# Kernel optimization log

Measured on AMD Instinct MI355X. Metric: run time of the kernel, lower is better.

The kernel has to match this reference:

```python
import jax, jax.numpy as jnp
import numpy as np

# channels_choice from the module: [8,16,24,32,40,48,56,64]
CH = jnp.arange(8, 72, 8)
EPS = 1e-5

def _masks():
    # [8,64] binary masks: mask[i, ch] = 1 if ch < channels_choice[i]
    return (jnp.arange(64)[None, :] < CH[:, None]).astype(jnp.float32)

def _bn(x, axes):
    # BatchNorm, affine=False, track_running_stats=False -> batch statistics
    mu = jnp.mean(x, axes, keepdims=True)
    var = jnp.var(x, axes, keepdims=True)
    return (x - mu) * jax.lax.rsqrt(var + EPS)

def _conv3(x, w):
    return jax.lax.conv_general_dilated(x, w, (1, 1), 'SAME',
                                        dimension_numbers=('NCHW', 'OIHW', 'NCHW'))

def _nor_conv(x, w1, w2, a1, a2):
    # Entangled two-part nor_conv edge.
    # p1: relu -> conv3x3 -> bn, mixture over 8 output-channel widths. Slicing
    # output channels + zero-pad + alpha-weighted sum collapses (BN is per-channel)
    # to a soft channel mask m1.
    masks = _masks()                      # [8,64]
    m1 = masks.T @ a1                     # [64] soft output-channel mask
    h = _bn(_conv3(jax.nn.relu(x), w1), (0, 2, 3)) * m1[None, :, None, None]
    # p2: conv3x3 -> bn, mixture over 8 input-channel widths. BN is nonlinear, so
    # the 8 candidates are genuinely computed (vectorized on a leading axis).
    xs = h[None] * masks[:, None, :, None, None]   # [8,B,64,H,W]
    K, B, C, H, W = xs.shape
    y = _conv3(xs.reshape(K * B, C, H, W), w2).reshape(K, B, C, H, W)
    y = _bn(y, (1, 3, 4))
    return jnp.einsum('k,kbchw->bchw', a2, y)

def _avg_pool3(x):
    # AvgPool2d(3, stride=1, padding=1, count_include_pad=False)
    s = jax.lax.reduce_window(x, 0.0, jax.lax.add, (1, 1, 3, 3), (1, 1, 1, 1), 'SAME')
    cnt = jax.lax.reduce_window(jnp.ones((1, 1) + x.shape[2:], x.dtype), 0.0,
                                jax.lax.add, (1, 1, 3, 3), (1, 1, 1, 1), 'SAME')
    return s / cnt

def _combi_mask(a1, a2):
    # combi=True mixture over itertools.product(channels, channels) with weights
    # a1[i]*a2[j]; for channelwise ops (skip/pool) slicing in to c_i then out to c_j
    # keeps channels < min(c_i,c_j), so the double sum factorizes into m1*m2.
    masks = _masks()
    return (masks.T @ a1) * (masks.T @ a2)

def _cell(inputs, alphas1, alphas2, W1_0, W2_0, W1_1, W2_1, W1_4, W2_4, W1_5, W2_5):
    cm = _combi_mask(alphas1, alphas2)[None, :, None, None]
    # genotype: 1<-(conv~0) | 2<-(conv~0, avgpool~1) | 3<-(skip~0, conv~1, conv~2)
    n1 = _nor_conv(inputs, W1_0, W2_0, alphas1, alphas2)
    n2 = _nor_conv(inputs, W1_1, W2_1, alphas1, alphas2) + _avg_pool3(n1) * cm
    n3 = (inputs * cm
          + _nor_conv(n1, W1_4, W2_4, alphas1, alphas2)
          + _nor_conv(n2, W1_5, W2_5, alphas1, alphas2))
    return n3

def setup_inputs():
    key = jax.random.key(0)
    ks = jax.random.split(key, 12)
    B, C, H, W = 64, 64, 32, 32
    a1 = jax.random.uniform(ks[1], (8,), jnp.float32)
    a2 = jax.random.uniform(ks[2], (8,), jnp.float32)
    d = {
        'inputs': jax.random.normal(ks[0], (B, C, H, W), jnp.float32),
        'alphas1': a1 / a1.sum(),
        'alphas2': a2 / a2.sum(),
    }
    wscale = 0.05  # ~ 1/sqrt(64*9) fan-in init
    for i, name in enumerate(['W1_0', 'W2_0', 'W1_1', 'W2_1', 'W1_4', 'W2_4', 'W1_5', 'W2_5']):
        d[name] = jax.random.normal(ks[3 + i], (64, 64, 3, 3), jnp.float32) * wscale
    return d

def reference(inputs, alphas1, alphas2, W1_0, W2_0, W1_1, W2_1, W1_4, W2_4, W1_5, W2_5):
    return _cell(inputs, alphas1, alphas2, W1_0, W2_0, W1_1, W2_1, W1_4, W2_4, W1_5, W2_5)
```

## Files before the change

kernel.cpp:

```cpp
#include <hip/hip_runtime.h>

#define EPS 1e-5f
#define NRED 65536.0f
#define IMST 73984
#define PATCH 8704
#define PATCH6 13056

typedef short bf16x8 __attribute__((ext_vector_type(8)));
typedef float f32x4 __attribute__((ext_vector_type(4)));
typedef unsigned short u16;

#define MFMA16(a, b, c) __builtin_amdgcn_mfma_f32_16x16x32_bf16(a, b, c, 0, 0, 0)
#define SWZ(px, oct) ((px) * 64 + (((oct) ^ ((px) & 7)) * 8))

__device__ __forceinline__ u16 f2bf(float x) {
  union { float f; unsigned u; } v; v.f = x;
  unsigned r = v.u + 0x7FFF + ((v.u >> 16) & 1);
  return (u16)(r >> 16);
}
__device__ __forceinline__ float bf2f(u16 h) {
  union { unsigned u; float f; } v; v.u = ((unsigned)h) << 16;
  return v.f;
}
__device__ __forceinline__ unsigned pk2(float a, float b) {
  return (unsigned)f2bf(a) | ((unsigned)f2bf(b) << 16);
}

template <int CTRL>
__device__ __forceinline__ float dpp_mov(float x) {
  int xi = __builtin_bit_cast(int, x);
  int r = __builtin_amdgcn_update_dpp(0, xi, CTRL, 0xF, 0xF, true);
  return __builtin_bit_cast(float, r);
}
__device__ __forceinline__ float row_reduce16(float x) {
  x += dpp_mov<0x111>(x);
  x += dpp_mov<0x112>(x);
  x += dpp_mov<0x114>(x);
  x += dpp_mov<0x118>(x);
  return x;
}

__device__ __forceinline__ void stage_mask(const u16* __restrict__ src,
                                           u16* __restrict__ shp, int tid, int R0) {
#pragma unroll
  for (int i = 0; i < 5; ++i) {
    int c = i * 256 + tid;
    if (i == 4 && tid >= 64) break;
    int px = c >> 3, oct = c & 7;
    int prow = px / 34, pcol = px - prow * 34;
    bool halo = (R0 + prow == 0) || (R0 + prow == 33) || (pcol == 0) || (pcol == 33);
    uint4 v = {0u, 0u, 0u, 0u};
    if (!halo) v = *(const uint4*)&src[(size_t)c * 8];
    *(uint4*)&shp[SWZ(px, oct)] = v;
  }
}

__device__ __forceinline__ void stage_affine(const u16* __restrict__ src,
                                             u16* __restrict__ shp, int tid, int R0,
                                             const float* __restrict__ stE) {
  const int oct0 = tid & 7;
  float s[8], bb[8];
#pragma unroll
  for (int j = 0; j < 8; ++j) { s[j] = stE[oct0 * 8 + j]; bb[j] = stE[64 + oct0 * 8 + j]; }
#pragma unroll
  for (int i = 0; i < 5; ++i) {
    int c = i * 256 + tid;
    if (i == 4 && tid >= 64) break;
    int px = c >> 3, oct = c & 7;
    int prow = px / 34, pcol = px - prow * 34;
    bool halo = (R0 + prow == 0) || (R0 + prow == 33) || (pcol == 0) || (pcol == 33);
    uint4 o = {0u, 0u, 0u, 0u};
    if (!halo) {
      uint4 u = *(const uint4*)&src[(size_t)c * 8];
      unsigned uv[4] = {u.x, u.y, u.z, u.w};
      unsigned rv[4];
#pragma unroll
      for (int p2 = 0; p2 < 4; ++p2) {
        float lo = bf2f((u16)(uv[p2] & 0xffff)) * s[p2 * 2] + bb[p2 * 2];
        float hi = bf2f((u16)(uv[p2] >> 16)) * s[p2 * 2 + 1] + bb[p2 * 2 + 1];
        rv[p2] = pk2(lo, hi);
      }
      o.x = rv[0]; o.y = rv[1]; o.z = rv[2]; o.w = rv[3];
    }
    *(uint4*)&shp[SWZ(px, oct)] = o;
  }
}


__global__ __launch_bounds__(256) void prep_k(
    const float* __restrict__ x, u16* __restrict__ xT, u16* __restrict__ n1T,
    const float* __restrict__ w10, const float* __restrict__ w11,
    const float* __restrict__ w12, const float* __restrict__ w13,
    const float* __restrict__ w20, const float* __restrict__ w21,
    const float* __restrict__ w22, const float* __restrict__ w23,
    u16* __restrict__ wT1, u16* __restrict__ wG64, u16* __restrict__ wT8) {
  __shared__ __align__(16) u16 sh[64 * 72];
  const int bid = blockIdx.x;
  const int tid = threadIdx.x;
  if (bid < 36) {
    int e = bid / 9, tap = bid % 9;
    const float* w = e == 0 ? w10 : e == 1 ? w11 : e == 2 ? w12 : w13;
    u16* dst = wT1 + e * 36864 + tap * 4096;
    for (int idx = tid; idx < 4096; idx += 256) {
      int co = idx >> 6, ci = idx & 63;
      dst[idx] = f2bf(w[(co * 64 + ci) * 9 + tap]);
    }
  } else if (bid < 324) {
    int r = bid - 36;
    int e = r / 72, bx = r % 72;
    const float* w = e == 0 ? w20 : e == 1 ? w21 : e == 2 ? w22 : w23;
    int g, tap;
    u16* dst;
    if (bx < 64) { g = bx >> 3; tap = bx & 7; dst = wG64 + e * 32768 + bx * 512; }
    else         { g = bx - 64; tap = 8;      dst = wT8 + e * 4096 + g * 512; }
    for (int idx = tid; idx < 512; idx += 256) {
      int co = idx >> 3, cig = idx & 7;
      dst[idx] = f2bf(w[(co * 64 + g * 8 + cig) * 9 + tap]);
    }
  } else if (bid < 388) {
    int b = bid - 324;
    if (tid >= 132) return;
    int R, C;
    if (tid < 34) { R = 0; C = tid; }
    else if (tid < 68) { R = 33; C = tid - 34; }
    else if (tid < 100) { R = tid - 67; C = 0; }
    else { R = tid - 99; C = 33; }
    u16* p = n1T + (size_t)b * IMST + (size_t)(R * 34 + C) * 64;
    uint4 z = {0u, 0u, 0u, 0u};
#pragma unroll
    for (int i = 0; i < 8; ++i) *(uint4*)&p[i * 8] = z;
  } else {
    const int bb = bid - 388;
    const int b = bb >> 4, slab = bb & 15;
    const int ln = tid & 63, w = tid >> 6;
    const float* xb = x + (size_t)b * 65536 + slab * 64;
#pragma unroll
    for (int i = 0; i < 16; ++i) {
      int ci = w + i * 4;
      float v = xb[ci * 1024 + ln];
      sh[ln * 72 + ci] = f2bf(fmaxf(v, 0.f));
    }
    __syncthreads();
    u16* dst = xT + (size_t)b * IMST;
#pragma unroll
    for (int j = 0; j < 2; ++j) {
      int idx = tid + j * 256;
      int p = idx >> 3, oct = idx & 7;
      int gp = slab * 64 + p;
      int R = gp >> 5, C = gp & 31;
      *(uint4*)&dst[((R + 1) * 34 + C + 1) * 64 + oct * 8] = *(const uint4*)&sh[p * 72 + oct * 8];
    }
  }
}

__global__ __launch_bounds__(256, 4) void convA_k(const u16* __restrict__ in0,
                                                  const u16* __restrict__ in1,
                                                  const u16* __restrict__ wTa,
                                                  const u16* __restrict__ wTb,
                                                  u16* __restrict__ t0,
                                                  u16* __restrict__ t1,
                                                  float* __restrict__ pA) {
  __shared__ __align__(16) u16 shp[PATCH];
  __shared__ float sA[64], qA[64];
  const int tid = threadIdx.x;
  const int b = blockIdx.y, R0 = blockIdx.x * 2, z = blockIdx.z;
  const u16* xin = z ? in1 : in0;
  const u16* wT = z ? wTb : wTa;
  u16* t = z ? t1 : t0;
  if (tid < 64) { sA[tid] = 0.f; qA[tid] = 0.f; }
  stage_mask(xin + (size_t)b * IMST + (size_t)R0 * 2176, shp, tid, R0);
  const int lane = tid & 63, w = tid >> 6;
  const int ln = lane & 15, quad = lane >> 4;
  const int lr = w >> 1, mh = w & 1;
  const u16* wbase = wT + (size_t)((mh * 2) * 16 + ln) * 64 + quad * 8;
  __syncthreads();
  f32x4 acc[2][2];
#pragma unroll
  for (int m2 = 0; m2 < 2; ++m2)
#pragma unroll
    for (int nf = 0; nf < 2; ++nf) acc[m2][nf] = (f32x4){0.f, 0.f, 0.f, 0.f};
#pragma unroll 3
  for (int tap = 0; tap < 9; ++tap) {
    const int dy = tap / 3, dx = tap % 3;
    const int px0 = (lr + dy) * 34 + ln + dx;
    bf16x8 A[2][2];
#pragma unroll
    for (int m2 = 0; m2 < 2; ++m2)
#pragma unroll
      for (int h = 0; h < 2; ++h)
        A[m2][h] = *(const bf16x8*)&wbase[(size_t)(tap * 64 + m2 * 16) * 64 + h * 32];
#pragma unroll
    for (int h = 0; h < 2; ++h) {
      const int oct = h * 4 + quad;
      bf16x8 b0 = *(const bf16x8*)&shp[SWZ(px0, oct)];
      bf16x8 b1 = *(const bf16x8*)&shp[SWZ(px0 + 16, oct)];
      acc[0][0] = MFMA16(A[0][h], b0, acc[0][0]);
      acc[0][1] = MFMA16(A[0][h], b1, acc[0][1]);
      acc[1][0] = MFMA16(A[1][h], b0, acc[1][0]);
      acc[1][1] = MFMA16(A[1][h], b1, acc[1][1]);
    }
  }
  const int R = R0 + lr;
#pragma unroll
  for (int m2 = 0; m2 < 2; ++m2) {
    const int cob = (mh * 2 + m2) * 16 + quad * 4;
#pragma unroll
    for (int nf = 0; nf < 2; ++nf) {
      u16* tb = t + (size_t)b * IMST + (size_t)((R + 1) * 34 + nf * 16 + ln + 1) * 64 + cob;
      uint2 pk;
      pk.x = pk2(acc[m2][nf][0], acc[m2][nf][1]);
      pk.y = pk2(acc[m2][nf][2], acc[m2][nf][3]);
      *(uint2*)tb = pk;
    }
#pragma unroll
    for (int r = 0; r < 4; ++r) {
      float v0 = acc[m2][0][r], v1 = acc[m2][1][r];
      float s = row_reduce16(v0) + row_reduce16(v1);
      float q = row_reduce16(v0 * v0) + row_reduce16(v1 * v1);
      if (ln == 15) {
        atomicAdd(&sA[cob + r], s);
        atomicAdd(&qA[cob + r], q);
      }
    }
  }
  __syncthreads();
  const int blk = z * 1024 + blockIdx.y * 16 + blockIdx.x;
  if (tid < 64) pA[blk * 128 + tid] = sA[tid];
  else if (tid < 128) pA[blk * 128 + tid] = qA[tid - 64];
}

__global__ __launch_bounds__(256) void reducerA_k(const float* __restrict__ pA,
                                                  const float* __restrict__ a1,
                                                  float* __restrict__ stBase) {
  const int tid = threadIdx.x, c = blockIdx.x, z = blockIdx.y;
  const float* pAe = pA + (size_t)z * 1024 * 128;
  float s = 0.f, q = 0.f;
  for (int i = tid; i < 1024; i += 256) {
    s += pAe[i * 128 + c];
    q += pAe[i * 128 + 64 + c];
  }
#pragma unroll
  for (int off = 32; off; off >>= 1) { s += __shfl_xor(s, off); q += __shfl_xor(q, off); }
  __shared__ float red[8];
  int wv = tid >> 6;
  if ((tid & 63) == 0) { red[wv] = s; red[4 + wv] = q; }
  __syncthreads();
  if (tid == 0) {
    float S = red[0] + red[1] + red[2] + red[3];
    float Q = red[4] + red[5] + red[6] + red[7];
    int g = c >> 3;
    float m = 0.f;
    for (int i = g; i < 8; ++i) m += a1[i];
    float mu = S * (1.f / NRED);
    float var = Q * (1.f / NRED) - mu * mu;
    float r = rsqrtf(var + EPS);
    float* stE = stBase + z * 2048;
    stE[c] = r * m;
    stE[64 + c] = -mu * r * m;
  }
}

__global__ __launch_bounds__(512, 4) void convC_k(const u16* __restrict__ t0,
                                                  const u16* __restrict__ t1,
                                                  const u16* __restrict__ wG64,
                                                  const u16* __restrict__ wT8,
                                                  const float* __restrict__ stBase,
                                                  float* __restrict__ pC) {
  __shared__ __align__(16) u16 shp[PATCH6];
  __shared__ __align__(16) u16 shA[64 * 16 * 8];
  __shared__ __align__(16) u16 shA2[8 * 16 * 8];
  __shared__ float sC[4][128], qC[4][128];
  const int tid = threadIdx.x;
  const int b = blockIdx.y, R0 = blockIdx.x * 4;
  const int edge = blockIdx.z;
  const u16* t = edge ? t1 : t0;
  const float* stE = stBase + edge * 2048;
  const u16* wGe = wG64 + edge * 32768;
  const u16* wT8e = wT8 + edge * 4096;
  ((float*)sC)[tid] = 0.f;
  ((float*)qC)[tid] = 0.f;
  {
    const int oct0 = tid & 7;
    float sc[8], bc[8];
#pragma unroll
    for (int j = 0; j < 8; ++j) { sc[j] = stE[oct0 * 8 + j]; bc[j] = stE[64 + oct0 * 8 + j]; }
    const u16* src = t + (size_t)b * IMST + (size_t)R0 * 2176;
#pragma unroll
    for (int i = 0; i < 4; ++i) {
      int c = i * 512 + tid;
      if (i == 3 && tid >= 96) break;
      int px = c >> 3, oct = c & 7;
      int prow = px / 34, pcol = px - prow * 34;
      bool halo = (R0 + prow == 0) || (R0 + prow == 33) || (pcol == 0) || (pcol == 33);
      uint4 o = {0u, 0u, 0u, 0u};
      if (!halo) {
        uint4 u = *(const uint4*)&src[(size_t)c * 8];
        unsigned uv[4] = {u.x, u.y, u.z, u.w};
        unsigned rv[4];
#pragma unroll
        for (int p2 = 0; p2 < 4; ++p2) {
          float lo = bf2f((u16)(uv[p2] & 0xffff)) * sc[p2 * 2] + bc[p2 * 2];
          float hi = bf2f((u16)(uv[p2] >> 16)) * sc[p2 * 2 + 1] + bc[p2 * 2 + 1];
          rv[p2] = pk2(lo, hi);
        }
        o.x = rv[0]; o.y = rv[1]; o.z = rv[2]; o.w = rv[3];
      }
      *(uint4*)&shp[SWZ(px, oct)] = o;
    }
  }
#pragma unroll
  for (int i = 0; i < 2; ++i) {
    int c = i * 512 + tid;
    int row = c >> 4, col = c & 15;
    *(uint4*)&shA[c * 8] = *(const uint4*)&wGe[(size_t)(row * 64 + col) * 8];
  }
  if (tid < 128) {
    int g = tid >> 4, col = tid & 15;
    *(uint4*)&shA2[tid * 8] = *(const uint4*)&wT8e[(size_t)(g * 64 + col) * 8];
  }
  __syncthreads();
  const int lane = tid & 63, w = tid >> 6;
  const int ln = lane & 15, quad = lane >> 4;
  const int lrow = w >> 1, colbase = (w & 1) * 16;
  int px[3];
#pragma unroll
  for (int ch = 0; ch < 3; ++ch) {
    int tp = ch * 4 + quad; if (tp > 8) tp = 8;
    px[ch] = (lrow + tp / 3) * 34 + colbase + ln + tp % 3;
  }
#pragma unroll 1
  for (int coq = 0; coq < 4; ++coq) {
    uint4 wr0, wr1, wr2;
    if (coq < 3) {
      const int nq = coq + 1;
      {
        int c = tid;
        wr0 = *(const uint4*)&wGe[(size_t)((c >> 4) * 64 + nq * 16 + (c & 15)) * 8];
      }
      {
        int c = 512 + tid;
        wr1 = *(const uint4*)&wGe[(size_t)((c >> 4) * 64 + nq * 16 + (c & 15)) * 8];
      }
      if (tid < 128)
        wr2 = *(const uint4*)&wT8e[(size_t)((tid >> 4) * 64 + nq * 16 + (tid & 15)) * 8];
    }
    f32x4 acc[8];
#pragma unroll
    for (int g = 0; g < 8; ++g) acc[g] = (f32x4){0.f, 0.f, 0.f, 0.f};
#pragma unroll
    for (int g = 0; g < 8; ++g) {
#pragma unroll
      for (int ch = 0; ch < 3; ++ch) {
        bf16x8 bx = *(const bf16x8*)&shp[SWZ(px[ch], g)];
        bf16x8 aw;
        if (ch < 2) {
          aw = *(const bf16x8*)&shA[((g * 8 + ch * 4 + quad) * 16 + ln) * 8];
        } else {
          aw = (bf16x8){0, 0, 0, 0, 0, 0, 0, 0};
          if (quad == 0) aw = *(const bf16x8*)&shA2[(g * 16 + ln) * 8];
        }
        acc[g] = MFMA16(aw, bx, acc[g]);
      }
    }
    f32x4 P = (f32x4){0.f, 0.f, 0.f, 0.f};
#pragma unroll
    for (int k = 0; k < 8; ++k) {
      P += acc[k];
#pragma unroll
      for (int r = 0; r < 4; ++r) {
        float v = P[r];
        float s = row_reduce16(v);
        float q = row_reduce16(v * v);
        if (ln == 15) {
          atomicAdd(&sC[coq][k * 16 + quad * 4 + r], s);
          atomicAdd(&qC[coq][k * 16 + quad * 4 + r], q);
        }
      }
    }
    __syncthreads();
    if (coq < 3) {
      *(uint4*)&shA[(size_t)tid * 8] = wr0;
      *(uint4*)&shA[(size_t)(512 + tid) * 8] = wr1;
      if (tid < 128) *(uint4*)&shA2[tid * 8] = wr2;
      __syncthreads();
    }
  }
  __syncthreads();
  const int blk = blockIdx.y * 8 + blockIdx.x;
#pragma unroll 1
  for (int coq = 0; coq < 4; ++coq) {
    const size_t base = ((size_t)(edge * 4 + coq) * 512 + blk) * 256;
    if (tid < 128) pC[base + tid] = sC[coq][tid];
    else if (tid < 256) pC[base + 128 + (tid - 128)] = qC[coq][tid - 128];
  }
}

__global__ __launch_bounds__(256) void redCprepE_k(const float* __restrict__ pC,
                                                   const float* __restrict__ w2a,
                                                   const float* __restrict__ w2b,
                                                   const float* __restrict__ a1,
                                                   const float* __restrict__ a2,
                                                   float* __restrict__ stBase,
                                                   u16* __restrict__ wEbase,
                                                   float* __restrict__ cm) {
  const int tid = threadIdx.x, c = blockIdx.x, z = blockIdx.y;
  const int coq = c >> 4, cl = c & 15;
  const float* w2 = z ? w2b : w2a;
  float* stE = stBase + z * 2048;
  u16* wE = wEbase + z * 36864;
  float s[8], q[8];
#pragma unroll
  for (int k = 0; k < 8; ++k) { s[k] = 0.f; q[k] = 0.f; }
  for (int i = tid; i < 512; i += 256) {
    const float* pb = pC + ((size_t)(z * 4 + coq) * 512 + i) * 256;
#pragma unroll
    for (int k = 0; k < 8; ++k) {
      s[k] += pb[k * 16 + cl];
      q[k] += pb[128 + k * 16 + cl];
    }
  }
#pragma unroll
  for (int k = 0; k < 8; ++k) {
#pragma unroll
    for (int off = 32; off; off >>= 1) { s[k] += __shfl_xor(s[k], off); q[k] += __shfl_xor(q[k], off); }
  }
  __shared__ float red[4][16];
  __shared__ float gL[8];
  int wv = tid >> 6;
  if ((tid & 63) == 0) {
#pragma unroll
    for (int k = 0; k < 8; ++k) { red[wv][k * 2] = s[k]; red[wv][k * 2 + 1] = q[k]; }
  }
  __syncthreads();
  if (tid == 0) {
    float suf = 0.f, bias = 0.f;
    for (int k = 7; k >= 0; --k) {
      float S = red[0][k * 2] + red[1][k * 2] + red[2][k * 2] + red[3][k * 2];
      float Q = red[0][k * 2 + 1] + red[1][k * 2 + 1] + red[2][k * 2 + 1] + red[3][k * 2 + 1];
      float mu = S * (1.f / NRED);
      float var = Q * (1.f / NRED) - mu * mu;
      float rr = rsqrtf(var + EPS);
      bias -= a2[k] * mu * rr;
      suf += a2[k] * rr;
      gL[k] = suf;
    }
    stE[128 + c] = bias;
    if (z == 0) {
      int g = c >> 3;
      float m1 = 0.f, m2 = 0.f;
      for (int i = g; i < 8; ++i) { m1 += a1[i]; m2 += a2[i]; }
      cm[c] = m1 * m2;
    }
  }
  __syncthreads();
  for (int idx = tid; idx < 576; idx += 256) {
    int tap = idx >> 6, ci = idx & 63;
    wE[(tap * 64 + c) * 64 + ci] = f2bf(w2[(c * 64 + ci) * 9 + tap] * gL[ci >> 3]);
  }
}

template <int MODE>
__global__ __launch_bounds__(256, 4) void convE_k(const u16* __restrict__ t,
                                                  const float* __restrict__ stE,
                                                  const u16* __restrict__ wEp,
                                                  u16* __restrict__ d1,
                                                  u16* __restrict__ d2,
                                                  const float* __restrict__ cm) {
  __shared__ __align__(16) u16 shp[PATCH];
  __shared__ __align__(16) u16 shn[MODE == 1 ? PATCH : 8];
  __shared__ float cmL[64], biasL[64];
  const int tid = threadIdx.x;
  const int b = blockIdx.y, R0 = blockIdx.x * 2;
  if (tid < 64) { cmL[tid] = cm[tid]; biasL[tid] = stE[128 + tid]; }
  stage_affine(t + (size_t)b * IMST + (size_t)R0 * 2176, shp, tid, R0, stE);
  if constexpr (MODE == 1) {
    const u16* nsrc = d2 + (size_t)b * IMST + (size_t)R0 * 2176;
#pragma unroll
    for (int i = 0; i < 5; ++i) {
      int c = i * 256 + tid;
      if (i == 4 && tid >= 64) break;
      int px = c >> 3, oct = c & 7;
      *(uint4*)&shn[SWZ(px, oct)] = *(const uint4*)&nsrc[(size_t)c * 8];
    }
  }
  const int lane = tid & 63, w = tid >> 6;
  const int ln = lane & 15, quad = lane >> 4;
  const int lr = w >> 1, mh = w & 1;
  const u16* wbase = wEp + (size_t)((mh * 2) * 16 + ln) * 64 + quad * 8;
  __syncthreads();
  f32x4 acc[2][2];
#pragma unroll
  for (int m2 = 0; m2 < 2; ++m2)
#pragma unroll
    for (int nf = 0; nf < 2; ++nf) acc[m2][nf] = (f32x4){0.f, 0.f, 0.f, 0.f};
#pragma unroll 3
  for (int tap = 0; tap < 9; ++tap) {
    const int dy = tap / 3, dx = tap % 3;
    const int px0 = (lr + dy) * 34 + ln + dx;
    bf16x8 A[2][2];
#pragma unroll
    for (int m2 = 0; m2 < 2; ++m2)
#pragma unroll
      for (int h = 0; h < 2; ++h)
        A[m2][h] = *(const bf16x8*)&wbase[(size_t)(tap * 64 + m2 * 16) * 64 + h * 32];
#pragma unroll
    for (int h = 0; h < 2; ++h) {
      const int oct = h * 4 + quad;
      bf16x8 b0 = *(const bf16x8*)&shp[SWZ(px0, oct)];
      bf16x8 b1 = *(const bf16x8*)&shp[SWZ(px0 + 16, oct)];
      acc[0][0] = MFMA16(A[0][h], b0, acc[0][0]);
      acc[0][1] = MFMA16(A[0][h], b1, acc[0][1]);
      acc[1][0] = MFMA16(A[1][h], b0, acc[1][0]);
      acc[1][1] = MFMA16(A[1][h], b1, acc[1][1]);
    }
  }
  const int R = R0 + lr;
#pragma unroll
  for (int m2 = 0; m2 < 2; ++m2) {
    const int cob = (mh * 2 + m2) * 16 + quad * 4;
#pragma unroll
    for (int nf = 0; nf < 2; ++nf) {
      const int C = nf * 16 + ln;
      const size_t haloPx = (size_t)b * IMST + (size_t)((R + 1) * 34 + C + 1) * 64 + cob;
      float v[4];
#pragma unroll
      for (int r = 0; r < 4; ++r) v[r] = acc[m2][nf][r] + biasL[cob + r];
      if (MODE == 0) {
        uint2 pk, pkr;
        pk.x = pk2(v[0], v[1]); pk.y = pk2(v[2], v[3]);
        pkr.x = pk2(fmaxf(v[0], 0.f), fmaxf(v[1], 0.f));
        pkr.y = pk2(fmaxf(v[2], 0.f), fmaxf(v[3], 0.f));
        *(uint2*)&d1[haloPx] = pk;
        *(uint2*)&d2[haloPx] = pkr;
      } else {
        float ps[4] = {0.f, 0.f, 0.f, 0.f};
#pragma unroll
        for (int dy = 0; dy < 3; ++dy)
#pragma unroll
          for (int dx = 0; dx < 3; ++dx) {
            const int ppx = (lr + dy) * 34 + C + dx;
            uint2 u = *(const uint2*)&shn[SWZ(ppx, cob >> 3) + (cob & 7)];
            ps[0] += bf2f((u16)(u.x & 0xffff));
            ps[1] += bf2f((u16)(u.x >> 16));
            ps[2] += bf2f((u16)(u.y & 0xffff));
            ps[3] += bf2f((u16)(u.y >> 16));
          }
        float rows = 3.f - (R == 0 ? 1.f : 0.f) - (R == 31 ? 1.f : 0.f);
        float cols = 3.f - (C == 0 ? 1.f : 0.f) - (C == 31 ? 1.f : 0.f);
        float inv = 1.f / (rows * cols);
        uint2 pkr;
        float t0v = fmaxf(v[0] + ps[0] * inv * cmL[cob], 0.f);
        float t1v = fmaxf(v[1] + ps[1] * inv * cmL[cob + 1], 0.f);
        float t2v = fmaxf(v[2] + ps[2] * inv * cmL[cob + 2], 0.f);
        float t3v = fmaxf(v[3] + ps[3] * inv * cmL[cob + 3], 0.f);
        pkr.x = pk2(t0v, t1v); pkr.y = pk2(t2v, t3v);
        *(uint2*)&d1[haloPx] = pkr;
      }
    }
  }
}

__global__ __launch_bounds__(256, 4) void convE23_k(const u16* __restrict__ t0,
                                                    const u16* __restrict__ t1,
                                                    const float* __restrict__ stBase,
                                                    const u16* __restrict__ wE2,
                                                    const u16* __restrict__ wE3,
                                                    float* __restrict__ outp,
                                                    const float* __restrict__ x,
                                                    const float* __restrict__ cm) {
  __shared__ __align__(16) u16 shp2[2 * PATCH];
  __shared__ float cmL[64], biasL[64];
  const int tid = threadIdx.x;
  const int b = blockIdx.y, R0 = blockIdx.x * 2;
  if (tid < 64) {
    cmL[tid] = cm[tid];
    biasL[tid] = stBase[128 + tid] + stBase[2048 + 128 + tid];
  }
  stage_affine(t0 + (size_t)b * IMST + (size_t)R0 * 2176, shp2, tid, R0, stBase);
  stage_affine(t1 + (size_t)b * IMST + (size_t)R0 * 2176, shp2 + PATCH, tid, R0, stBase + 2048);
  __syncthreads();
  const int lane = tid & 63, w = tid >> 6;
  const int ln = lane & 15, quad = lane >> 4;
  const int lr = w >> 1, mh = w & 1;
  f32x4 acc[2][2];
#pragma unroll
  for (int m2 = 0; m2 < 2; ++m2)
#pragma unroll
    for (int nf = 0; nf < 2; ++nf) acc[m2][nf] = (f32x4){0.f, 0.f, 0.f, 0.f};
#pragma unroll 1
  for (int ei = 0; ei < 2; ++ei) {
    const u16* wEp = ei ? wE3 : wE2;
    const u16* sp = &shp2[ei * PATCH];
    const u16* wbase = wEp + (size_t)((mh * 2) * 16 + ln) * 64 + quad * 8;
#pragma unroll 3
    for (int tap = 0; tap < 9; ++tap) {
      const int dy = tap / 3, dx = tap % 3;
      const int px0 = (lr + dy) * 34 + ln + dx;
      bf16x8 A[2][2];
#pragma unroll
      for (int m2 = 0; m2 < 2; ++m2)
#pragma unroll
        for (int h = 0; h < 2; ++h)
          A[m2][h] = *(const bf16x8*)&wbase[(size_t)(tap * 64 + m2 * 16) * 64 + h * 32];
#pragma unroll
      for (int h = 0; h < 2; ++h) {
        const int oct = h * 4 + quad;
        bf16x8 b0 = *(const bf16x8*)&sp[SWZ(px0, oct)];
        bf16x8 b1 = *(const bf16x8*)&sp[SWZ(px0 + 16, oct)];
        acc[0][0] = MFMA16(A[0][h], b0, acc[0][0]);
        acc[0][1] = MFMA16(A[0][h], b1, acc[0][1]);
        acc[1][0] = MFMA16(A[1][h], b0, acc[1][0]);
        acc[1][1] = MFMA16(A[1][h], b1, acc[1][1]);
      }
    }
  }
  const int R = R0 + lr;
#pragma unroll
  for (int m2 = 0; m2 < 2; ++m2) {
    const int cob = (mh * 2 + m2) * 16 + quad * 4;
#pragma unroll
    for (int nf = 0; nf < 2; ++nf) {
      const int C = nf * 16 + ln;
      size_t base = (size_t)b * 65536 + (size_t)cob * 1024 + R * 32 + C;
#pragma unroll
      for (int r = 0; r < 4; ++r)
        outp[base + (size_t)r * 1024] =
            acc[m2][nf][r] + biasL[cob + r] + x[base + (size_t)r * 1024] * cmL[cob + r];
    }
  }
}

extern "C" void kernel_launch(void* const* d_in, const int* in_sizes, int n_in,
                              void* d_out, int out_size, void* d_ws, size_t ws_size,
                              hipStream_t stream) {
  const float* x  = (const float*)d_in[0];
  const float* a1 = (const float*)d_in[1];
  const float* a2 = (const float*)d_in[2];
  const float* W1[4] = {(const float*)d_in[3], (const float*)d_in[5],
                        (const float*)d_in[7], (const float*)d_in[9]};
  const float* W2[4] = {(const float*)d_in[4], (const float*)d_in[6],
                        (const float*)d_in[8], (const float*)d_in[10]};
  float* out = (float*)d_out;
  char* ws = (char*)d_ws;
  const size_t HB = (size_t)IMST * 64 * 2;
  u16* xT  = (u16*)ws;
  u16* t0  = (u16*)(ws + HB);
  u16* t1  = (u16*)(ws + 2 * HB);
  u16* n1T = (u16*)(ws + 3 * HB);
  u16* n1r = (u16*)(ws + 4 * HB);
  u16* n2r = (u16*)(ws + 5 * HB);
  char* p = ws + 6 * HB;
  float* st  = (float*)p;            p += 8256 * 4;
  u16* wT1   = (u16*)p;              p += 4 * 36864 * 2;
  u16* wG64  = (u16*)p;              p += 4 * 32768 * 2;
  u16* wT8   = (u16*)p;              p += 4 * 4096 * 2;
  u16* wE    = (u16*)p;              p += 4 * 36864 * 2;
  float* pA  = (float*)p;            p += 2 * 1024 * 128 * 4;
  float* pC  = (float*)p;
  float* cm  = st + 8192;

  prep_k<<<1412, 256, 0, stream>>>(x, xT, n1T,
                                   W1[0], W1[1], W1[2], W1[3],
                                   W2[0], W2[1], W2[2], W2[3],
                                   wT1, wG64, wT8);

  dim3 gA(16, 64, 2), gC(8, 64, 2), gE(16, 64);
  convA_k<<<gA, 256, 0, stream>>>(xT, xT, wT1, wT1 + 36864, t0, t1, pA);
  reducerA_k<<<dim3(64, 2), 256, 0, stream>>>(pA, a1, st);
  convC_k<<<gC, 512, 0, stream>>>(t0, t1, wG64, wT8, st, pC);
  redCprepE_k<<<dim3(64, 2), 256, 0, stream>>>(pC, W2[0], W2[1], a1, a2, st, wE, cm);
  convE_k<0><<<gE, 256, 0, stream>>>(t0, st, wE, n1T, n1r, cm);
  convE_k<1><<<gE, 256, 0, stream>>>(t1, st + 2048, wE + 36864, n2r, n1T, cm);
  convA_k<<<gA, 256, 0, stream>>>(n1r, n2r, wT1 + 2 * 36864, wT1 + 3 * 36864, t0, t1, pA);
  reducerA_k<<<dim3(64, 2), 256, 0, stream>>>(pA, a1, st + 4096);
  convC_k<<<gC, 512, 0, stream>>>(t0, t1, wG64 + 2 * 32768, wT8 + 2 * 4096, st + 4096, pC);
  redCprepE_k<<<dim3(64, 2), 256, 0, stream>>>(pC, W2[2], W2[3], a1, a2, st + 4096,
                                               wE + 2 * 36864, cm);
  convE23_k<<<gE, 256, 0, stream>>>(t0, t1, st + 4096, wE + 2 * 36864, wE + 3 * 36864,
                                    out, x, cm);
}
```

Baseline: 423.4 us.

## Fuse n1 and n2 convE stages, recomputing n1 halo rows in shared memory

Merges the two convE launches into one kernel. Each block now computes the raw n1 output for its two rows plus one halo row above and below, keeps it in shared memory, and uses it directly for the avg-pool term of n2. This drops the n1T global round trip, the n1T halo zeroing in prep, and one kernel launch. The cost is redundant conv work on the halo rows, which doubles the MFMA work for the n1 part, plus larger shared memory that lowers occupancy from 4 to 3 blocks per SIMD.

Measured after the change: 449.4 us. 6.2% more time.

```diff
diff --git a/kernel.cpp b/kernel.cpp
--- a/kernel.cpp
+++ b/kernel.cpp
@@ -88,7 +88,7 @@
 
 
 __global__ __launch_bounds__(256) void prep_k(
-    const float* __restrict__ x, u16* __restrict__ xT, u16* __restrict__ n1T,
+    const float* __restrict__ x, u16* __restrict__ xT,
     const float* __restrict__ w10, const float* __restrict__ w11,
     const float* __restrict__ w12, const float* __restrict__ w13,
     const float* __restrict__ w20, const float* __restrict__ w21,
@@ -117,20 +117,8 @@
       int co = idx >> 3, cig = idx & 7;
       dst[idx] = f2bf(w[(co * 64 + g * 8 + cig) * 9 + tap]);
     }
-  } else if (bid < 388) {
-    int b = bid - 324;
-    if (tid >= 132) return;
-    int R, C;
-    if (tid < 34) { R = 0; C = tid; }
-    else if (tid < 68) { R = 33; C = tid - 34; }
-    else if (tid < 100) { R = tid - 67; C = 0; }
-    else { R = tid - 99; C = 33; }
-    u16* p = n1T + (size_t)b * IMST + (size_t)(R * 34 + C) * 64;
-    uint4 z = {0u, 0u, 0u, 0u};
-#pragma unroll
-    for (int i = 0; i < 8; ++i) *(uint4*)&p[i * 8] = z;
   } else {
-    const int bb = bid - 388;
+    const int bb = bid - 324;
     const int b = bb >> 4, slab = bb & 15;
     const int ln = tid & 63, w = tid >> 6;
     const float* xb = x + (size_t)b * 65536 + slab * 64;
@@ -459,34 +447,122 @@
   }
 }
 
-template <int MODE>
-__global__ __launch_bounds__(256, 4) void convE_k(const u16* __restrict__ t,
-                                                  const float* __restrict__ stE,
-                                                  const u16* __restrict__ wEp,
-                                                  u16* __restrict__ d1,
-                                                  u16* __restrict__ d2,
-                                                  const float* __restrict__ cm) {
-  __shared__ __align__(16) u16 shp[PATCH];
-  __shared__ __align__(16) u16 shn[MODE == 1 ? PATCH : 8];
-  __shared__ float cmL[64], biasL[64];
+__global__ __launch_bounds__(256, 3) void convE01_k(const u16* __restrict__ t0,
+                                                    const u16* __restrict__ t1,
+                                                    const float* __restrict__ stBase,
+                                                    const u16* __restrict__ wE1,
+                                                    const u16* __restrict__ wE2,
+                                                    u16* __restrict__ n1r,
+                                                    u16* __restrict__ n2r,
+                                                    const float* __restrict__ cm) {
+  __shared__ __align__(16) u16 shp6[PATCH6];
+  __shared__ __align__(16) u16 shn[PATCH];
+  __shared__ float cmL[64], b0L[64], b1L[64];
   const int tid = threadIdx.x;
   const int b = blockIdx.y, R0 = blockIdx.x * 2;
-  if (tid < 64) { cmL[tid] = cm[tid]; biasL[tid] = stE[128 + tid]; }
-  stage_affine(t + (size_t)b * IMST + (size_t)R0 * 2176, shp, tid, R0, stE);
-  if constexpr (MODE == 1) {
-    const u16* nsrc = d2 + (size_t)b * IMST + (size_t)R0 * 2176;
-#pragma unroll
-    for (int i = 0; i < 5; ++i) {
+  if (tid < 64) {
+    cmL[tid] = cm[tid];
+    b0L[tid] = stBase[128 + tid];
+    b1L[tid] = stBase[2048 + 128 + tid];
+  }
+  {
+    const int oct0 = tid & 7;
+    float sc[8], bc[8];
+#pragma unroll
+    for (int j = 0; j < 8; ++j) { sc[j] = stBase[oct0 * 8 + j]; bc[j] = stBase[64 + oct0 * 8 + j]; }
+    const int S = R0 - 1;
+    const u16* src = t0 + (size_t)b * IMST + (ptrdiff_t)S * 2176;
+#pragma unroll
+    for (int i = 0; i < 7; ++i) {
       int c = i * 256 + tid;
-      if (i == 4 && tid >= 64) break;
+      if (i == 6 && tid >= 96) break;
       int px = c >> 3, oct = c & 7;
-      *(uint4*)&shn[SWZ(px, oct)] = *(const uint4*)&nsrc[(size_t)c * 8];
+      int prow = px / 34, pcol = px - prow * 34;
+      int ar = S + prow;
+      bool halo = (ar <= 0) || (ar >= 33) || (pcol == 0) || (pcol == 33);
+      uint4 o = {0u, 0u, 0u, 0u};
+      if (!halo) {
+        uint4 u = *(const uint4*)&src[(size_t)c * 8];
+        unsigned uv[4] = {u.x, u.y, u.z, u.w};
+        unsigned rv[4];
+#pragma unroll
+        for (int p2 = 0; p2 < 4; ++p2) {
+          float lo = bf2f((u16)(uv[p2] & 0xffff)) * sc[p2 * 2] + bc[p2 * 2];
+          float hi = bf2f((u16)(uv[p2] >> 16)) * sc[p2 * 2 + 1] + bc[p2 * 2 + 1];
+          rv[p2] = pk2(lo, hi);
+        }
+        o.x = rv[0]; o.y = rv[1]; o.z = rv[2]; o.w = rv[3];
+      }
+      *(uint4*)&shp6[SWZ(px, oct)] = o;
     }
   }
   const int lane = tid & 63, w = tid >> 6;
   const int ln = lane & 15, quad = lane >> 4;
   const int lr = w >> 1, mh = w & 1;
-  const u16* wbase = wEp + (size_t)((mh * 2) * 16 + ln) * 64 + quad * 8;
+  if (tid < 64) {
+    int rr = tid >> 4, colsel = (tid >> 3) & 1, oct = tid & 7;
+    uint4 z = {0u, 0u, 0u, 0u};
+    *(uint4*)&shn[SWZ(rr * 34 + (colsel ? 33 : 0), oct)] = z;
+  }
+  const u16* wb1 = wE1 + (size_t)((mh * 2) * 16 + ln) * 64 + quad * 8;
+  const u16* wb2 = wE2 + (size_t)((mh * 2) * 16 + ln) * 64 + quad * 8;
+  __syncthreads();
+#pragma unroll 1
+  for (int ri = 0; ri < 2; ++ri) {
+    const int nr = 2 * ri + lr;
+    const int orow = R0 - 1 + nr;
+    f32x4 acc[2][2];
+#pragma unroll
+    for (int m2 = 0; m2 < 2; ++m2)
+#pragma unroll
+      for (int nf = 0; nf < 2; ++nf) acc[m2][nf] = (f32x4){0.f, 0.f, 0.f, 0.f};
+#pragma unroll 3
+    for (int tap = 0; tap < 9; ++tap) {
+      const int dy = tap / 3, dx = tap % 3;
+      const int px0 = (nr + dy) * 34 + ln + dx;
+      bf16x8 A[2][2];
+#pragma unroll
+      for (int m2 = 0; m2 < 2; ++m2)
+#pragma unroll
+        for (int h = 0; h < 2; ++h)
+          A[m2][h] = *(const bf16x8*)&wb1[(size_t)(tap * 64 + m2 * 16) * 64 + h * 32];
+#pragma unroll
+      for (int h = 0; h < 2; ++h) {
+        const int oct = h * 4 + quad;
+        bf16x8 b0 = *(const bf16x8*)&shp6[SWZ(px0, oct)];
+        bf16x8 b1 = *(const bf16x8*)&shp6[SWZ(px0 + 16, oct)];
+        acc[0][0] = MFMA16(A[0][h], b0, acc[0][0]);
+        acc[0][1] = MFMA16(A[0][h], b1, acc[0][1]);
+        acc[1][0] = MFMA16(A[1][h], b0, acc[1][0]);
+        acc[1][1] = MFMA16(A[1][h], b1, acc[1][1]);
+      }
+    }
+    const bool valid = (orow >= 0) && (orow <= 31);
+    const bool interior = (nr == 1) || (nr == 2);
+#pragma unroll
+    for (int m2 = 0; m2 < 2; ++m2) {
+      const int cob = (mh * 2 + m2) * 16 + quad * 4;
+#pragma unroll
+      for (int nf = 0; nf < 2; ++nf) {
+        const int C = nf * 16 + ln;
+        float v[4];
+#pragma unroll
+        for (int r = 0; r < 4; ++r) v[r] = acc[m2][nf][r] + b0L[cob + r];
+        uint2 raw;
+        raw.x = pk2(v[0], v[1]); raw.y = pk2(v[2], v[3]);
+        if (!valid) { raw.x = 0u; raw.y = 0u; }
+        *(uint2*)&shn[SWZ(nr * 34 + C + 1, cob >> 3) + (cob & 7)] = raw;
+        if (interior) {
+          uint2 pr;
+          pr.x = pk2(fmaxf(v[0], 0.f), fmaxf(v[1], 0.f));
+          pr.y = pk2(fmaxf(v[2], 0.f), fmaxf(v[3], 0.f));
+          *(uint2*)&n1r[(size_t)b * IMST + (size_t)((orow + 1) * 34 + C + 1) * 64 + cob] = pr;
+        }
+      }
+    }
+  }
+  __syncthreads();
+  stage_affine(t1 + (size_t)b * IMST + (size_t)R0 * 2176, shp6, tid, R0, stBase + 2048);
   __syncthreads();
   f32x4 acc[2][2];
 #pragma unroll
@@ -502,12 +578,12 @@
     for (int m2 = 0; m2 < 2; ++m2)
 #pragma unroll
       for (int h = 0; h < 2; ++h)
-        A[m2][h] = *(const bf16x8*)&wbase[(size_t)(tap * 64 + m2 * 16) * 64 + h * 32];
+        A[m2][h] = *(const bf16x8*)&wb2[(size_t)(tap * 64 + m2 * 16) * 64 + h * 32];
 #pragma unroll
     for (int h = 0; h < 2; ++h) {
       const int oct = h * 4 + quad;
-      bf16x8 b0 = *(const bf16x8*)&shp[SWZ(px0, oct)];
-      bf16x8 b1 = *(const bf16x8*)&shp[SWZ(px0 + 16, oct)];
+      bf16x8 b0 = *(const bf16x8*)&shp6[SWZ(px0, oct)];
+      bf16x8 b1 = *(const bf16x8*)&shp6[SWZ(px0 + 16, oct)];
       acc[0][0] = MFMA16(A[0][h], b0, acc[0][0]);
       acc[0][1] = MFMA16(A[0][h], b1, acc[0][1]);
       acc[1][0] = MFMA16(A[1][h], b0, acc[1][0]);
@@ -524,38 +600,29 @@
       const size_t haloPx = (size_t)b * IMST + (size_t)((R + 1) * 34 + C + 1) * 64 + cob;
       float v[4];
 #pragma unroll
-      for (int r = 0; r < 4; ++r) v[r] = acc[m2][nf][r] + biasL[cob + r];
-      if (MODE == 0) {
-        uint2 pk, pkr;
-        pk.x = pk2(v[0], v[1]); pk.y = pk2(v[2], v[3]);
-        pkr.x = pk2(fmaxf(v[0], 0.f), fmaxf(v[1], 0.f));
-        pkr.y = pk2(fmaxf(v[2], 0.f), fmaxf(v[3], 0.f));
-        *(uint2*)&d1[haloPx] = pk;
-        *(uint2*)&d2[haloPx] = pkr;
-      } else {
-        float ps[4] = {0.f, 0.f, 0.f, 0.f};
-#pragma unroll
-        for (int dy = 0; dy < 3; ++dy)
-#pragma unroll
-          for (int dx = 0; dx < 3; ++dx) {
-            const int ppx = (lr + dy) * 34 + C + dx;
-            uint2 u = *(const uint2*)&shn[SWZ(ppx, cob >> 3) + (cob & 7)];
-            ps[0] += bf2f((u16)(u.x & 0xffff));
-            ps[1] += bf2f((u16)(u.x >> 16));
-            ps[2] += bf2f((u16)(u.y & 0xffff));
-            ps[3] += bf2f((u16)(u.y >> 16));
-          }
-        float rows = 3.f - (R == 0 ? 1.f : 0.f) - (R == 31 ? 1.f : 0.f);
-        float cols = 3.f - (C == 0 ? 1.f : 0.f) - (C == 31 ? 1.f : 0.f);
-        float inv = 1.f / (rows * cols);
-        uint2 pkr;
-        float t0v = fmaxf(v[0] + ps[0] * inv * cmL[cob], 0.f);
-        float t1v = fmaxf(v[1] + ps[1] * inv * cmL[cob + 1], 0.f);
-        float t2v = fmaxf(v[2] + ps[2] * inv * cmL[cob + 2], 0.f);
-        float t3v = fmaxf(v[3] + ps[3] * inv * cmL[cob + 3], 0.f);
-        pkr.x = pk2(t0v, t1v); pkr.y = pk2(t2v, t3v);
-        *(uint2*)&d1[haloPx] = pkr;
-      }
+      for (int r = 0; r < 4; ++r) v[r] = acc[m2][nf][r] + b1L[cob + r];
+      float ps[4] = {0.f, 0.f, 0.f, 0.f};
+#pragma unroll
+      for (int dy = 0; dy < 3; ++dy)
+#pragma unroll
+        for (int dx = 0; dx < 3; ++dx) {
+          const int ppx = (lr + dy) * 34 + C + dx;
+          uint2 u = *(const uint2*)&shn[SWZ(ppx, cob >> 3) + (cob & 7)];
+          ps[0] += bf2f((u16)(u.x & 0xffff));
+          ps[1] += bf2f((u16)(u.x >> 16));
+          ps[2] += bf2f((u16)(u.y & 0xffff));
+          ps[3] += bf2f((u16)(u.y >> 16));
+        }
+      float rows = 3.f - (R == 0 ? 1.f : 0.f) - (R == 31 ? 1.f : 0.f);
+      float cols = 3.f - (C == 0 ? 1.f : 0.f) - (C == 31 ? 1.f : 0.f);
+      float inv = 1.f / (rows * cols);
+      uint2 pkr;
+      float t0v = fmaxf(v[0] + ps[0] * inv * cmL[cob], 0.f);
+      float t1v = fmaxf(v[1] + ps[1] * inv * cmL[cob + 1], 0.f);
+      float t2v = fmaxf(v[2] + ps[2] * inv * cmL[cob + 2], 0.f);
+      float t3v = fmaxf(v[3] + ps[3] * inv * cmL[cob + 3], 0.f);
+      pkr.x = pk2(t0v, t1v); pkr.y = pk2(t2v, t3v);
+      *(uint2*)&n2r[haloPx] = pkr;
     }
   }
 }
@@ -646,7 +713,6 @@
   u16* xT  = (u16*)ws;
   u16* t0  = (u16*)(ws + HB);
   u16* t1  = (u16*)(ws + 2 * HB);
-  u16* n1T = (u16*)(ws + 3 * HB);
   u16* n1r = (u16*)(ws + 4 * HB);
   u16* n2r = (u16*)(ws + 5 * HB);
   char* p = ws + 6 * HB;
@@ -659,7 +725,7 @@
   float* pC  = (float*)p;
   float* cm  = st + 8192;
 
-  prep_k<<<1412, 256, 0, stream>>>(x, xT, n1T,
+  prep_k<<<1348, 256, 0, stream>>>(x, xT,
                                    W1[0], W1[1], W1[2], W1[3],
                                    W2[0], W2[1], W2[2], W2[3],
                                    wT1, wG64, wT8);
@@ -669,8 +735,7 @@
   reducerA_k<<<dim3(64, 2), 256, 0, stream>>>(pA, a1, st);
   convC_k<<<gC, 512, 0, stream>>>(t0, t1, wG64, wT8, st, pC);
   redCprepE_k<<<dim3(64, 2), 256, 0, stream>>>(pC, W2[0], W2[1], a1, a2, st, wE, cm);
-  convE_k<0><<<gE, 256, 0, stream>>>(t0, st, wE, n1T, n1r, cm);
-  convE_k<1><<<gE, 256, 0, stream>>>(t1, st + 2048, wE + 36864, n2r, n1T, cm);
+  convE01_k<<<gE, 256, 0, stream>>>(t0, t1, st, wE, wE + 36864, n1r, n2r, cm);
   convA_k<<<gA, 256, 0, stream>>>(n1r, n2r, wT1 + 2 * 36864, wT1 + 3 * 36864, t0, t1, pA);
   reducerA_k<<<dim3(64, 2), 256, 0, stream>>>(pA, a1, st + 4096);
   convC_k<<<gC, 512, 0, stream>>>(t0, t1, wG64 + 2 * 32768, wT8 + 2 * 4096, st + 4096, pC);
```
